# Kernel tuning notes

Hardware: AMD Instinct MI355X
Metric: run time of the kernel (lower is better)

Reference implementation:

```python
import jax, jax.numpy as jnp
import numpy as np

B, T_SUB, L, H, K = 64, 512, 256, 1024, 9


def setup_inputs() -> dict:
    key = jax.random.key(0)
    ks = jax.random.split(key, 8)
    sequence_output = jax.random.normal(ks[0], (B, T_SUB, H), jnp.float32)
    attention_mask = jnp.ones((B, T_SUB), jnp.int32)
    offsets = jnp.sort(jax.random.randint(ks[1], (B, L), 0, T_SUB), axis=1)
    mask = jnp.ones((B, L), bool)
    labels = jax.random.randint(ks[2], (B, L), 0, K)
    classifier_w = jax.random.normal(ks[3], (H, K), jnp.float32) / np.sqrt(H).astype(np.float32)
    classifier_b = jnp.zeros((K,), jnp.float32)
    start_transitions = jax.random.uniform(ks[4], (K,), jnp.float32, -0.1, 0.1)
    end_transitions = jax.random.uniform(ks[5], (K,), jnp.float32, -0.1, 0.1)
    transitions = jax.random.uniform(ks[6], (K, K), jnp.float32, -0.1, 0.1)
    return {
        'sequence_output': sequence_output, 'attention_mask': attention_mask,
        'offsets': offsets, 'mask': mask, 'labels': labels,
        'classifier_w': classifier_w, 'classifier_b': classifier_b,
        'start_transitions': start_transitions, 'end_transitions': end_transitions,
        'transitions': transitions,
    }


def crf_log_likelihood(emissions, tags, mask_b, start, trans, end):
    # emissions [B,L,K], tags [B,L] int, mask_b [B,L] bool (mask[:,0] all True)
    maskf = mask_b.astype(emissions.dtype)
    # numerator: score of the gold path
    first_tag = tags[:, 0]
    score = start[first_tag] + jnp.take_along_axis(emissions[:, 0], first_tag[:, None], 1)[:, 0]
    trans_sc = trans[tags[:, :-1], tags[:, 1:]]                                   # [B,L-1]
    emit_sc = jnp.take_along_axis(emissions[:, 1:], tags[:, 1:, None], 2)[..., 0]  # [B,L-1]
    score = score + jnp.sum((trans_sc + emit_sc) * maskf[:, 1:], axis=1)
    seq_ends = jnp.sum(mask_b.astype(jnp.int32), axis=1) - 1
    last_tags = jnp.take_along_axis(tags, seq_ends[:, None], 1)[:, 0]
    score = score + end[last_tags]
    # denominator: log partition via scan over time
    def step(alpha, xs):
        em_i, m_i = xs  # [B,K], [B]
        nxt = jax.nn.logsumexp(alpha[:, :, None] + trans[None] + em_i[:, None, :], axis=1)
        return jnp.where(m_i[:, None], nxt, alpha), None
    alpha0 = start[None] + emissions[:, 0]
    xs = (jnp.swapaxes(emissions[:, 1:], 0, 1), jnp.swapaxes(mask_b[:, 1:], 0, 1))
    alphaL, _ = jax.lax.scan(step, alpha0, xs)
    denom = jax.nn.logsumexp(alphaL + end[None], axis=1)
    return score - denom


def crf_viterbi(emissions, mask_b, start, trans, end):
    k = emissions.shape[-1]
    iden = jnp.arange(k)[None, :]
    def step(score, xs):
        em_i, m_i = xs
        cand = score[:, :, None] + trans[None]     # [B,K_prev,K_cur]
        idx = jnp.argmax(cand, axis=1)             # [B,K]
        nxt = jnp.max(cand, axis=1) + em_i
        score = jnp.where(m_i[:, None], nxt, score)
        idx = jnp.where(m_i[:, None], idx, iden)   # identity through padding
        return score, idx
    score0 = start[None] + emissions[:, 0]
    xs = (jnp.swapaxes(emissions[:, 1:], 0, 1), jnp.swapaxes(mask_b[:, 1:], 0, 1))
    final, hist = jax.lax.scan(step, score0, xs)   # hist [L-1,B,K]
    last = jnp.argmax(final + end[None], axis=1)   # [B]
    def back(tag, h):
        prev = jnp.take_along_axis(h, tag[:, None], 1)[:, 0]
        return prev, tag
    tag0, ys = jax.lax.scan(back, last, hist, reverse=True)  # ys[i] = tag_{i+1}
    path = jnp.concatenate([tag0[None], ys], axis=0)          # [L,B]
    return jnp.swapaxes(path, 0, 1)


def reference(sequence_output, attention_mask, offsets, mask, labels,
              classifier_w, classifier_b, start_transitions, end_transitions, transitions):
    # embedder: sub_token_mode='first' -> gather first-subtoken embedding per word
    embed = jnp.take_along_axis(sequence_output, offsets[:, :, None], axis=1)  # [B,L,H]
    # dropout is identity at inference
    logits = embed @ classifier_w + classifier_b                               # [B,L,K]
    crf_mask = mask                                                            # word-level CRF mask
    tags = labels * crf_mask.astype(labels.dtype)
    llh = crf_log_likelihood(logits, tags, crf_mask, start_transitions, transitions, end_transitions)
    loss = -jnp.mean(llh)
    predicts = crf_viterbi(logits, crf_mask, start_transitions, transitions, end_transitions)
    predicts = predicts * crf_mask.astype(predicts.dtype)
    return loss, logits, predicts
```

## Files before the change

### kernel.cpp

```cpp
#include <hip/hip_runtime.h>
#include <math.h>

#define BB 64
#define TSUB 512
#define LL 256
#define HH 1024
#define KK 9

#define S_CHUNK 37
#define N_CHUNK 7

#define HQ 128
#define NQ 8
#define ROWS_PB 64
#define TILE (KK * ROWS_PB)
#define NBLK (BB * TSUB / ROWS_PB * NQ)
#define P_TOTAL (NBLK * TILE)

__device__ __forceinline__ float bcast(float v, int lane) {
    return __int_as_float(__builtin_amdgcn_readlane(__float_as_int(v), lane));
}
__device__ __forceinline__ float fexp2(float x) { return __builtin_amdgcn_exp2f(x); }
__device__ __forceinline__ float flog2(float x) { return __builtin_amdgcn_logf(x); }

__global__ __launch_bounds__(256) void logits_dense_kernel(
    const float* __restrict__ seq,
    const float* __restrict__ w,
    float*       __restrict__ part,
    int*         __restrict__ counter)
{
    if (blockIdx.x == 0 && threadIdx.x == 0)
        __hip_atomic_store(counter, 0, __ATOMIC_RELAXED, __HIP_MEMORY_SCOPE_AGENT);

    __shared__ float w_s[KK][HQ];
    const int tid = threadIdx.x;
    const int q     = blockIdx.x & (NQ - 1);
    const int group = blockIdx.x >> 3;

    const int wave = tid >> 6;
    const int lane = tid & 63;
    const int r_local = lane >> 2;
    const int s = lane & 3;

    const int rl  = wave * 16 + r_local;
    const int row = group * ROWS_PB + rl;
    const float* __restrict__ src = seq + (size_t)row * HH + q * HQ + s * 4;

    float4 x0 = *(const float4*)(src +   0);
    float4 x1 = *(const float4*)(src +  16);
    float4 x2 = *(const float4*)(src +  32);
    float4 x3 = *(const float4*)(src +  48);
    float4 x4 = *(const float4*)(src +  64);
    float4 x5 = *(const float4*)(src +  80);
    float4 x6 = *(const float4*)(src +  96);
    float4 x7 = *(const float4*)(src + 112);

    for (int i = tid; i < HQ * KK; i += 256) {
        int h = i / KK, k = i - h * KK;
        w_s[k][h] = w[q * (HQ * KK) + i];
    }
    __syncthreads();

    float acc[KK];
#pragma unroll
    for (int k = 0; k < KK; ++k) acc[k] = 0.0f;

#define FMA_STEP(ii, X)                                                   \
    {                                                                     \
        const int h0 = (ii) * 16 + s * 4;                                 \
        _Pragma("unroll")                                                 \
        for (int k = 0; k < KK; ++k) {                                    \
            float4 wv = *(const float4*)&w_s[k][h0];                      \
            acc[k] += X.x * wv.x + X.y * wv.y + X.z * wv.z + X.w * wv.w;  \
        }                                                                 \
    }
    FMA_STEP(0, x0)
    FMA_STEP(1, x1)
    FMA_STEP(2, x2)
    FMA_STEP(3, x3)
    FMA_STEP(4, x4)
    FMA_STEP(5, x5)
    FMA_STEP(6, x6)
    FMA_STEP(7, x7)
#undef FMA_STEP

#pragma unroll
    for (int k = 0; k < KK; ++k) {
        float a = acc[k];
        a += __shfl_xor(a, 1, 64);
        a += __shfl_xor(a, 2, 64);
        acc[k] = a;
    }

    __syncthreads();
    float* tile = &w_s[0][0];
#pragma unroll
    for (int jj = 0; jj < 3; ++jj) {
        const int k = s + 4 * jj;
        if (k < KK) tile[k * ROWS_PB + rl] = acc[k];
    }
    __syncthreads();

    float* __restrict__ dst = part + (size_t)blockIdx.x * TILE;
    if (tid < TILE / 4)
        *(float4*)(dst + tid * 4) = *(const float4*)(tile + tid * 4);
}

__global__ __launch_bounds__(256) void crf_kernel(
    const float* __restrict__ part,
    const int*   __restrict__ offsets,
    const int*   __restrict__ labels,
    const float* __restrict__ bias,
    const float* __restrict__ start_t,
    const float* __restrict__ end_t,
    const float* __restrict__ trans,
    float*       __restrict__ loss_out,
    float*       __restrict__ logits,
    float*       __restrict__ predicts,
    float*       __restrict__ llh_ws,
    int*         __restrict__ counter)
{
    __shared__ float em_all[TSUB * KK];
    __shared__ float em2[LL * KK];
    __shared__ int   s_off[LL];
    __shared__ int   lab[LL];
    __shared__ int   hist[(LL - 1) * KK];
    __shared__ int   path[LL];
    __shared__ float s_trans[KK * KK];
    __shared__ float s_bias[KK];
    __shared__ int   Fmap[N_CHUNK * KK];
    __shared__ int   s_bnd[N_CHUNK + 1];
    __shared__ float s_denom, s_score;
    __shared__ int   s_last;

    const float LOG2E = 1.4426950408889634f;
    const float LN2   = 0.6931471805599453f;

    const int b = blockIdx.x;
    const int tid = threadIdx.x;
    const size_t base_off = (size_t)b * LL * KK;

    if (tid < KK * KK) s_trans[tid] = trans[tid];
    if (tid < KK) s_bias[tid] = bias[tid];
    if (tid < LL / 4) {
        int4 lv = *(const int4*)(labels + b * LL + tid * 4);
        lab[tid * 4 + 0] = lv.x;
        lab[tid * 4 + 1] = lv.y;
        lab[tid * 4 + 2] = lv.z;
        lab[tid * 4 + 3] = lv.w;
        int4 ov = *(const int4*)(offsets + b * LL + tid * 4);
        s_off[tid * 4 + 0] = ov.x;
        s_off[tid * 4 + 1] = ov.y;
        s_off[tid * 4 + 2] = ov.z;
        s_off[tid * 4 + 3] = ov.w;
    }
    __syncthreads();

    for (int i = tid; i < KK * TSUB; i += 256) {
        const int k = i >> 9;
        const int t = i & (TSUB - 1);
        const int g = t >> 6;
        const int r = t & (ROWS_PB - 1);
        const float* __restrict__ pb =
            part + (size_t)((b * 8 + g) * NQ) * TILE + k * ROWS_PB + r;
        float v = s_bias[k];
#pragma unroll
        for (int qq = 0; qq < NQ; ++qq)
            v += pb[qq * TILE];
        em_all[t * KK + k] = v;
    }
    __syncthreads();

    for (int i = tid; i < LL * KK; i += 256) {
        const int l = i / KK, k = i - l * KK;
        float v = em_all[s_off[l] * KK + k];
        logits[base_off + i] = v;
        em2[i] = v * LOG2E;
    }
    __syncthreads();

    const int wave = tid >> 6;
    const int lane = tid & 63;
    const int j = (lane < KK) ? lane : 0;

    if (wave == 0) {
        float tcol2[KK], dt2[KK];
#pragma unroll
        for (int i = 0; i < KK; ++i) tcol2[i] = s_trans[i * KK + j] * LOG2E;
#pragma unroll
        for (int i = 1; i < KK; ++i) dt2[i] = tcol2[i] - tcol2[0];
        const float endj2 = end_t[j] * LOG2E;

        float a2 = start_t[j] * LOG2E + em2[j];
        float emv = em2[KK + j];
        for (int t = 1; t < LL; ++t) {
            float em_cur = emv;
            if (t + 1 < LL) emv = em2[(t + 1) * KK + j];
            float sa0 = bcast(a2, 0);
            float d = a2 - sa0;
            float qv[KK];
#pragma unroll
            for (int i = 1; i < KK; ++i) qv[i] = bcast(d, i) + dt2[i];
            float e1 = fexp2(qv[1]), e2 = fexp2(qv[2]);
            float e3 = fexp2(qv[3]), e4 = fexp2(qv[4]);
            float e5 = fexp2(qv[5]), e6 = fexp2(qv[6]);
            float e7 = fexp2(qv[7]), e8 = fexp2(qv[8]);
            float sum = (((e1 + e2) + (e3 + e4)) + ((e5 + e6) + (e7 + e8))) + 1.0f;
            a2 = sa0 + tcol2[0] + flog2(sum) + em_cur;
        }
        float v = a2 + endj2;
        float c[KK];
#pragma unroll
        for (int i = 0; i < KK; ++i) c[i] = bcast(v, i);
        float m = c[0];
#pragma unroll
        for (int i = 1; i < KK; ++i) m = fmaxf(m, c[i]);
        float sum = 0.0f;
#pragma unroll
        for (int i = 0; i < KK; ++i) sum += fexp2(c[i] - m);
        if (lane == 0) s_denom = (m + flog2(sum)) * LN2;
    } else if (wave == 1) {
        float tcol2[KK];
#pragma unroll
        for (int i = 0; i < KK; ++i) tcol2[i] = s_trans[i * KK + j] * LOG2E;
        const float endj2 = end_t[j] * LOG2E;

        float vs = start_t[j] * LOG2E + em2[j];
        float emv = em2[KK + j];
        for (int t = 1; t < LL; ++t) {
            float em_cur = emv;
            if (t + 1 < LL) emv = em2[(t + 1) * KK + j];
            float cand[KK];
#pragma unroll
            for (int i = 0; i < KK; ++i) cand[i] = bcast(vs, i) + tcol2[i];
            float m = fmaxf(fmaxf(fmaxf(cand[0], cand[1]), cand[2]),
                     fmaxf(fmaxf(fmaxf(cand[3], cand[4]), cand[5]),
                           fmaxf(fmaxf(cand[6], cand[7]), cand[8])));
            vs = m + em_cur;
            int bi = KK - 1;
#pragma unroll
            for (int i = KK - 2; i >= 0; --i) bi = (cand[i] == m) ? i : bi;
            hist[(t - 1) * KK + j] = bi;
        }
        float v = vs + endj2;
        float c[KK];
#pragma unroll
        for (int i = 0; i < KK; ++i) c[i] = bcast(v, i);
        float bv = c[0];
        int last = 0;
#pragma unroll
        for (int i = 1; i < KK; ++i) { if (c[i] > bv) { bv = c[i]; last = i; } }

        if (lane < N_CHUNK * KK) {
            const int cid = lane / KK;
            const int jj  = lane - cid * KK;
            const int lo = cid * S_CHUNK;
            int hi = lo + S_CHUNK;
            if (hi > LL - 1) hi = LL - 1;
            hi -= 1;
            int f = jj;
            for (int r = hi; r >= lo; --r) f = hist[r * KK + f];
            Fmap[cid * KK + jj] = f;
        }
        if (lane == 0) {
            s_bnd[N_CHUNK] = last;
            int st = last;
            for (int c2 = N_CHUNK - 1; c2 >= 0; --c2) {
                st = Fmap[c2 * KK + st];
                s_bnd[c2] = st;
            }
        }
        if (lane < N_CHUNK) {
            const int lo = lane * S_CHUNK;
            int hi = lo + S_CHUNK;
            if (hi > LL - 1) hi = LL - 1;
            hi -= 1;
            int x = s_bnd[lane + 1];
            for (int r = hi; r >= lo; --r) {
                x = hist[r * KK + x];
                path[r] = x;
            }
        }
        if (lane == 0) path[LL - 1] = last;
    } else if (wave == 2) {
        float part_s = 0.0f;
        for (int t = 1 + lane; t < LL; t += 64) {
            int tp = lab[t - 1], tc = lab[t];
            part_s += s_trans[tp * KK + tc] + em2[t * KK + tc] * LN2;
        }
#pragma unroll
        for (int d = 32; d; d >>= 1) part_s += __shfl_xor(part_s, d, 64);
        if (lane == 0) {
            int t0 = lab[0], tl = lab[LL - 1];
            s_score = part_s + start_t[t0] + em2[t0] * LN2 + end_t[tl];
        }
    }
    __syncthreads();

    for (int i = tid; i < LL; i += 256)
        predicts[b * LL + i] = (float)path[i];

    if (tid == 0) {
        float llh = s_score - s_denom;
        __hip_atomic_store(&llh_ws[b], llh, __ATOMIC_RELEASE,
                           __HIP_MEMORY_SCOPE_AGENT);
        int old = __hip_atomic_fetch_add(counter, 1, __ATOMIC_ACQ_REL,
                                         __HIP_MEMORY_SCOPE_AGENT);
        s_last = (old == BB - 1) ? 1 : 0;
    }
    __syncthreads();
    if (s_last && wave == 0) {
        float v = __hip_atomic_load(&llh_ws[lane], __ATOMIC_ACQUIRE,
                                    __HIP_MEMORY_SCOPE_AGENT);
#pragma unroll
        for (int d = 32; d; d >>= 1) v += __shfl_xor(v, d, 64);
        if (lane == 0) loss_out[0] = -v / (float)BB;
    }
}

extern "C" void kernel_launch(void* const* d_in, const int* in_sizes, int n_in,
                              void* d_out, int out_size, void* d_ws, size_t ws_size,
                              hipStream_t stream)
{
    (void)in_sizes; (void)n_in; (void)out_size; (void)ws_size;

    const float* seq     = (const float*)d_in[0];
    const int*   offsets = (const int*)d_in[2];
    const int*   labels  = (const int*)d_in[4];
    const float* w       = (const float*)d_in[5];
    const float* bias    = (const float*)d_in[6];
    const float* start_t = (const float*)d_in[7];
    const float* end_t   = (const float*)d_in[8];
    const float* trans   = (const float*)d_in[9];

    float* out      = (float*)d_out;
    float* logits   = out + 1;
    float* predicts = out + 1 + BB * LL * KK;

    float* part    = (float*)d_ws;
    float* llh_ws  = part + (size_t)P_TOTAL;
    int*   counter = (int*)(llh_ws + BB + 16);

    logits_dense_kernel<<<NBLK, 256, 0, stream>>>(seq, w, part, counter);
    crf_kernel<<<BB, 256, 0, stream>>>(part, offsets, labels, bias, start_t,
                                       end_t, trans, out, logits, predicts,
                                       llh_ws, counter);
}
```

Before: 251.3 us.

## Compute full hidden dimension per block and drop split-K partial buffer

The logits kernel now has each block cover all 1024 hidden channels for 64 rows, instead of splitting H into 8 quarter-blocks. The full weight matrix is staged in shared memory, and input loads are double-buffered across 128-wide chunks. Bias is added in the epilogue and the finished emissions are written in [t,k] layout, so the CRF kernel only copies them with float4 loads instead of summing 8 partials. This removes the partial-sum write/read traffic but cuts the grid to 512 blocks and raises LDS use to about 37KB per block, which may lower occupancy and latency hiding.

```diff
diff --git a/kernel.cpp b/kernel.cpp
--- a/kernel.cpp
+++ b/kernel.cpp
@@ -10,12 +10,11 @@
 #define S_CHUNK 37
 #define N_CHUNK 7
 
-#define HQ 128
-#define NQ 8
 #define ROWS_PB 64
-#define TILE (KK * ROWS_PB)
-#define NBLK (BB * TSUB / ROWS_PB * NQ)
-#define P_TOTAL (NBLK * TILE)
+#define NBLK (BB * TSUB / ROWS_PB)
+#define TILE (ROWS_PB * KK)
+#define EM_TOTAL (BB * TSUB * KK)
+#define WPAD 1032
 
 __device__ __forceinline__ float bcast(float v, int lane) {
     return __int_as_float(__builtin_amdgcn_readlane(__float_as_int(v), lane));
@@ -23,41 +22,35 @@
 __device__ __forceinline__ float fexp2(float x) { return __builtin_amdgcn_exp2f(x); }
 __device__ __forceinline__ float flog2(float x) { return __builtin_amdgcn_logf(x); }
 
-__global__ __launch_bounds__(256) void logits_dense_kernel(
+__global__ __launch_bounds__(256) void logits_full_kernel(
     const float* __restrict__ seq,
     const float* __restrict__ w,
-    float*       __restrict__ part,
+    const float* __restrict__ bias,
+    float*       __restrict__ em,
     int*         __restrict__ counter)
 {
     if (blockIdx.x == 0 && threadIdx.x == 0)
         __hip_atomic_store(counter, 0, __ATOMIC_RELAXED, __HIP_MEMORY_SCOPE_AGENT);
 
-    __shared__ float w_s[KK][HQ];
+    __shared__ float w_s[KK][WPAD];
     const int tid = threadIdx.x;
-    const int q     = blockIdx.x & (NQ - 1);
-    const int group = blockIdx.x >> 3;
-
     const int wave = tid >> 6;
     const int lane = tid & 63;
     const int r_local = lane >> 2;
     const int s = lane & 3;
 
     const int rl  = wave * 16 + r_local;
-    const int row = group * ROWS_PB + rl;
-    const float* __restrict__ src = seq + (size_t)row * HH + q * HQ + s * 4;
-
-    float4 x0 = *(const float4*)(src +   0);
-    float4 x1 = *(const float4*)(src +  16);
-    float4 x2 = *(const float4*)(src +  32);
-    float4 x3 = *(const float4*)(src +  48);
-    float4 x4 = *(const float4*)(src +  64);
-    float4 x5 = *(const float4*)(src +  80);
-    float4 x6 = *(const float4*)(src +  96);
-    float4 x7 = *(const float4*)(src + 112);
-
-    for (int i = tid; i < HQ * KK; i += 256) {
+    const int row = blockIdx.x * ROWS_PB + rl;
+    const float* __restrict__ src = seq + (size_t)row * HH + s * 4;
+
+    float4 xa[8], xb[8];
+#pragma unroll
+    for (int ii = 0; ii < 8; ++ii)
+        xa[ii] = *(const float4*)(src + ii * 16);
+
+    for (int i = tid; i < HH * KK; i += 256) {
         int h = i / KK, k = i - h * KK;
-        w_s[k][h] = w[q * (HQ * KK) + i];
+        w_s[k][h] = w[i];
     }
     __syncthreads();
 
@@ -65,24 +58,33 @@
 #pragma unroll
     for (int k = 0; k < KK; ++k) acc[k] = 0.0f;
 
-#define FMA_STEP(ii, X)                                                   \
-    {                                                                     \
-        const int h0 = (ii) * 16 + s * 4;                                 \
-        _Pragma("unroll")                                                 \
-        for (int k = 0; k < KK; ++k) {                                    \
-            float4 wv = *(const float4*)&w_s[k][h0];                      \
-            acc[k] += X.x * wv.x + X.y * wv.y + X.z * wv.z + X.w * wv.w;  \
-        }                                                                 \
-    }
-    FMA_STEP(0, x0)
-    FMA_STEP(1, x1)
-    FMA_STEP(2, x2)
-    FMA_STEP(3, x3)
-    FMA_STEP(4, x4)
-    FMA_STEP(5, x5)
-    FMA_STEP(6, x6)
-    FMA_STEP(7, x7)
-#undef FMA_STEP
+#define CHUNK_STEP(CUR, NXT, C, LAST)                                         \
+    {                                                                         \
+        if (!(LAST)) {                                                        \
+            _Pragma("unroll")                                                 \
+            for (int ii = 0; ii < 8; ++ii)                                    \
+                NXT[ii] = *(const float4*)(src + ((C) + 1) * 128 + ii * 16);  \
+        }                                                                     \
+        _Pragma("unroll")                                                     \
+        for (int ii = 0; ii < 8; ++ii) {                                      \
+            const int h0 = (C) * 128 + ii * 16 + s * 4;                       \
+            _Pragma("unroll")                                                 \
+            for (int k = 0; k < KK; ++k) {                                    \
+                float4 wv = *(const float4*)&w_s[k][h0];                      \
+                acc[k] += CUR[ii].x * wv.x + CUR[ii].y * wv.y                 \
+                        + CUR[ii].z * wv.z + CUR[ii].w * wv.w;                \
+            }                                                                 \
+        }                                                                     \
+    }
+    CHUNK_STEP(xa, xb, 0, 0)
+    CHUNK_STEP(xb, xa, 1, 0)
+    CHUNK_STEP(xa, xb, 2, 0)
+    CHUNK_STEP(xb, xa, 3, 0)
+    CHUNK_STEP(xa, xb, 4, 0)
+    CHUNK_STEP(xb, xa, 5, 0)
+    CHUNK_STEP(xa, xb, 6, 0)
+    CHUNK_STEP(xb, xa, 7, 1)
+#undef CHUNK_STEP
 
 #pragma unroll
     for (int k = 0; k < KK; ++k) {
@@ -97,20 +99,19 @@
 #pragma unroll
     for (int jj = 0; jj < 3; ++jj) {
         const int k = s + 4 * jj;
-        if (k < KK) tile[k * ROWS_PB + rl] = acc[k];
-    }
-    __syncthreads();
-
-    float* __restrict__ dst = part + (size_t)blockIdx.x * TILE;
+        if (k < KK) tile[rl * KK + k] = acc[k] + bias[k];
+    }
+    __syncthreads();
+
+    float* __restrict__ dst = em + (size_t)blockIdx.x * TILE;
     if (tid < TILE / 4)
         *(float4*)(dst + tid * 4) = *(const float4*)(tile + tid * 4);
 }
 
 __global__ __launch_bounds__(256) void crf_kernel(
-    const float* __restrict__ part,
+    const float* __restrict__ em,
     const int*   __restrict__ offsets,
     const int*   __restrict__ labels,
-    const float* __restrict__ bias,
     const float* __restrict__ start_t,
     const float* __restrict__ end_t,
     const float* __restrict__ trans,
@@ -127,7 +128,6 @@
     __shared__ int   hist[(LL - 1) * KK];
     __shared__ int   path[LL];
     __shared__ float s_trans[KK * KK];
-    __shared__ float s_bias[KK];
     __shared__ int   Fmap[N_CHUNK * KK];
     __shared__ int   s_bnd[N_CHUNK + 1];
     __shared__ float s_denom, s_score;
@@ -141,7 +141,6 @@
     const size_t base_off = (size_t)b * LL * KK;
 
     if (tid < KK * KK) s_trans[tid] = trans[tid];
-    if (tid < KK) s_bias[tid] = bias[tid];
     if (tid < LL / 4) {
         int4 lv = *(const int4*)(labels + b * LL + tid * 4);
         lab[tid * 4 + 0] = lv.x;
@@ -154,20 +153,13 @@
         s_off[tid * 4 + 2] = ov.z;
         s_off[tid * 4 + 3] = ov.w;
     }
-    __syncthreads();
-
-    for (int i = tid; i < KK * TSUB; i += 256) {
-        const int k = i >> 9;
-        const int t = i & (TSUB - 1);
-        const int g = t >> 6;
-        const int r = t & (ROWS_PB - 1);
-        const float* __restrict__ pb =
-            part + (size_t)((b * 8 + g) * NQ) * TILE + k * ROWS_PB + r;
-        float v = s_bias[k];
-#pragma unroll
-        for (int qq = 0; qq < NQ; ++qq)
-            v += pb[qq * TILE];
-        em_all[t * KK + k] = v;
+
+    {
+        const float* __restrict__ src = em + (size_t)b * TSUB * KK;
+        for (int i4 = tid; i4 < TSUB * KK / 4; i4 += 256) {
+            float4 v = *(const float4*)(src + i4 * 4);
+            *(float4*)&em_all[i4 * 4] = v;
+        }
     }
     __syncthreads();
 
@@ -337,12 +329,12 @@
     float* logits   = out + 1;
     float* predicts = out + 1 + BB * LL * KK;
 
-    float* part    = (float*)d_ws;
-    float* llh_ws  = part + (size_t)P_TOTAL;
+    float* em      = (float*)d_ws;
+    float* llh_ws  = em + (size_t)EM_TOTAL;
     int*   counter = (int*)(llh_ws + BB + 16);
 
-    logits_dense_kernel<<<NBLK, 256, 0, stream>>>(seq, w, part, counter);
-    crf_kernel<<<BB, 256, 0, stream>>>(part, offsets, labels, bias, start_t,
-                                       end_t, trans, out, logits, predicts,
+    logits_full_kernel<<<NBLK, 256, 0, stream>>>(seq, w, bias, em, counter);
+    crf_kernel<<<BB, 256, 0, stream>>>(em, offsets, labels, start_t, end_t,
+                                       trans, out, logits, predicts,
                                        llh_ws, counter);
 }
```

New measurement: 250.1 us. No clear change (-0.5%).
